# Kernel optimization log

Measured on AMD Instinct MI355X. Metric: run time of the kernel, lower is better.

The kernel has to match this reference:

```python
import jax, jax.numpy as jnp
import numpy as np


def _graph_conv(feat, W, b, src, dst, num_nodes):
    """DGL GraphConv with norm='both', activation=relu.
    out = relu(D_in^{-1/2} * A * D_out^{-1/2} * (X @ W) + b)
    Degrees are clamped to a minimum of 1 (DGL behavior).
    """
    # Linear transform first (d_in == d_out here, order is math-equivalent)
    h = feat @ W  # [N, d_out]
    ones = jnp.ones(src.shape[0], dtype=feat.dtype)
    out_deg = jnp.clip(jax.ops.segment_sum(ones, src, num_segments=num_nodes), 1.0)
    in_deg = jnp.clip(jax.ops.segment_sum(ones, dst, num_segments=num_nodes), 1.0)
    norm_src = jax.lax.rsqrt(out_deg)  # [N]
    norm_dst = jax.lax.rsqrt(in_deg)   # [N]
    # gather messages from source nodes, scaled by src norm
    msg = h[src] * norm_src[src][:, None]  # [E, d_out]
    agg = jax.ops.segment_sum(msg, dst, num_segments=num_nodes)  # [N, d_out]
    return jax.nn.relu(agg * norm_dst[:, None] + b)


def setup_inputs() -> dict:
    key = jax.random.key(0)
    ks = jax.random.split(key, 8)
    N = 50000
    E_c, E_d = 1600000, 800000
    d_c, d_d = 128, 256
    feat_c = jax.random.normal(ks[0], (N, d_c), dtype=jnp.float32)
    feat_d = jax.random.normal(ks[1], (N, d_d), dtype=jnp.float32)
    src_c = jax.random.randint(ks[2], (E_c,), 0, N, dtype=jnp.int32)
    dst_c = jax.random.randint(ks[3], (E_c,), 0, N, dtype=jnp.int32)
    src_d = jax.random.randint(ks[4], (E_d,), 0, N, dtype=jnp.int32)
    dst_d = jax.random.randint(ks[5], (E_d,), 0, N, dtype=jnp.int32)
    W_c = jax.random.normal(ks[6], (d_c, d_c), dtype=jnp.float32) * (1.0 / np.sqrt(d_c))
    W_d = jax.random.normal(ks[7], (d_d, d_d), dtype=jnp.float32) * (1.0 / np.sqrt(d_d))
    b_c = jnp.zeros((d_c,), dtype=jnp.float32)
    b_d = jnp.zeros((d_d,), dtype=jnp.float32)
    return {"feat_c": feat_c, "feat_d": feat_d, "src_c": src_c, "dst_c": dst_c,
            "src_d": src_d, "dst_d": dst_d, "W_c": W_c, "b_c": b_c,
            "W_d": W_d, "b_d": b_d}


def reference(feat_c, feat_d, src_c, dst_c, src_d, dst_d, W_c, b_c, W_d, b_d):
    N_c = feat_c.shape[0]
    N_d = feat_d.shape[0]
    homo_feature_c = _graph_conv(feat_c, W_c, b_c, src_c, dst_c, N_c)
    homo_feature_d = _graph_conv(feat_d, W_d, b_d, src_d, dst_d, N_d)
    return (homo_feature_c, homo_feature_d)
```

## Files before the change

kernel.cpp:

```cpp
#include <hip/hip_runtime.h>
#include <hip/hip_bf16.h>


typedef __attribute__((ext_vector_type(8))) short short8;
typedef __attribute__((ext_vector_type(4))) float f32x4;

#define RND 4096
#define CAPMAX 8960

static __device__ __forceinline__ ushort f2b(float f) {
    __hip_bfloat16 h = __float2bfloat16(f);
    return *reinterpret_cast<ushort*>(&h);
}
static __device__ __forceinline__ float b2f(ushort u) {
    union { unsigned int i; float f; } c;
    c.i = ((unsigned int)u) << 16;
    return c.f;
}
static __device__ __forceinline__ void gld_lds16(const void* g, void* l) {
    __builtin_amdgcn_global_load_lds(
        (const __attribute__((address_space(1))) unsigned int*)g,
        (__attribute__((address_space(3))) unsigned int*)l, 16, 0, 0);
}

__global__ __launch_bounds__(256) void part_kernel(
    const int* __restrict__ src_c, const int* __restrict__ dst_c, int Ec, int Rc,
    const int* __restrict__ src_d, const int* __restrict__ dst_d, int Ed, int Rd,
    int* gf_cd, int* gf_cs, int* gf_dd, int* gf_ds,
    int* dbuf_c, int* sbuf_c, int* dbuf_d, int* sbuf_d, int capc, int capd)
{
    __shared__ int pk[RND];
    __shared__ unsigned char pb[RND];
    __shared__ int hist[256], st[256], ex2[256], cur[256], gbase[256];

    const int tid = threadIdx.x;
    const int bid = blockIdx.x;
    const int* keys; const int* pays; int E; int* gf; int* buf; int cap; int e0;
    if (bid < Rc)            { keys = dst_c; pays = src_c; E = Ec; gf = gf_cd; buf = dbuf_c; cap = capc; e0 = bid * RND; }
    else if (bid < 2 * Rc)   { keys = src_c; pays = 0;     E = Ec; gf = gf_cs; buf = sbuf_c; cap = capc; e0 = (bid - Rc) * RND; }
    else if (bid < 2 * Rc + Rd) { keys = dst_d; pays = src_d; E = Ed; gf = gf_dd; buf = dbuf_d; cap = capd; e0 = (bid - 2 * Rc) * RND; }
    else                     { keys = src_d; pays = 0;     E = Ed; gf = gf_ds; buf = sbuf_d; cap = capd; e0 = (bid - 2 * Rc - Rd) * RND; }

    hist[tid] = 0;
    __syncthreads();

    int kb[RND / 256], pv[RND / 256];
    int n = 0;
#pragma unroll
    for (int r = 0; r < RND / 256; ++r) {
        int e = e0 + r * 256 + tid;
        if (e < E) {
            int k = keys[e];
            pv[r] = pays ? ((pays[e] << 8) | (k & 255)) : k;
            kb[r] = k >> 8;
            atomicAdd(&hist[kb[r]], 1);
            n = r + 1;
        }
    }
    __syncthreads();

    int x = hist[tid];
    st[tid] = x;
    __syncthreads();
    for (int off = 1; off < 256; off <<= 1) {
        int t2 = 0;
        if (tid >= off) t2 = st[tid - off];
        __syncthreads();
        if (tid >= off) st[tid] += t2;
        __syncthreads();
    }
    ex2[tid] = st[tid] - x;
    cur[tid] = st[tid] - x;
    __syncthreads();

    for (int r = 0; r < n; ++r) {
        int slot = atomicAdd(&cur[kb[r]], 1);
        pk[slot] = pv[r];
        pb[slot] = (unsigned char)kb[r];
    }
    if (x) gbase[tid] = atomicAdd(&gf[tid], x);
    __syncthreads();

    int m = st[255];
    for (int i = tid; i < m; i += 256) {
        int b = pb[i];
        int pos = gbase[b] + (i - ex2[b]);
        if (pos < cap) buf[(size_t)b * cap + pos] = pk[i];
    }
}

__global__ __launch_bounds__(256) void b2s_kernel(
    const int* __restrict__ sbuf_c, const int* __restrict__ gf_cs, int capc, int* cnt_c,
    const int* __restrict__ sbuf_d, const int* __restrict__ gf_ds, int capd, int* cnt_d,
    int N, int NBKT)
{
    __shared__ int h[256];
    const int tid = threadIdx.x;
    const int* sbuf; const int* gf; int cap; int* cnt; int bb;
    if ((int)blockIdx.x < NBKT) { sbuf = sbuf_c; gf = gf_cs; cap = capc; cnt = cnt_c; bb = blockIdx.x; }
    else { sbuf = sbuf_d; gf = gf_ds; cap = capd; cnt = cnt_d; bb = blockIdx.x - NBKT; }
    h[tid] = 0;
    __syncthreads();
    int m = gf[bb]; if (m > cap) m = cap;
    const int* reg = sbuf + (size_t)bb * cap;
    for (int i = tid; i < m; i += 256) atomicAdd(&h[reg[i] & 255], 1);
    __syncthreads();
    int v = bb * 256 + tid;
    if (v < N) cnt[v] = h[tid];
}

__global__ __launch_bounds__(256) void b2d_kernel(
    int* dbuf_c, const int* __restrict__ gf_cd, int capc, int* rs_c, int* dg_c,
    int* dbuf_d, const int* __restrict__ gf_dd, int capd, int* rs_d, int* dg_d,
    int N, int NBKT)
{
    __shared__ int pk[CAPMAX];
    __shared__ int h[256], st[256], ex2[256], cur[256];
    const int tid = threadIdx.x;
    int* bbuf; const int* gf; int cap; int* rs; int* dg; int bb;
    if ((int)blockIdx.x < NBKT) { bbuf = dbuf_c; gf = gf_cd; cap = capc; rs = rs_c; dg = dg_c; bb = blockIdx.x; }
    else { bbuf = dbuf_d; gf = gf_dd; cap = capd; rs = rs_d; dg = dg_d; bb = blockIdx.x - NBKT; }

    int m = gf[bb]; if (m > cap) m = cap;
    int* reg = bbuf + (size_t)bb * cap;

    h[tid] = 0;
    __syncthreads();
    for (int i = tid; i < m; i += 256) atomicAdd(&h[reg[i] & 255], 1);
    __syncthreads();
    int x = h[tid];
    st[tid] = x;
    __syncthreads();
    for (int off = 1; off < 256; off <<= 1) {
        int t2 = 0;
        if (tid >= off) t2 = st[tid - off];
        __syncthreads();
        if (tid >= off) st[tid] += t2;
        __syncthreads();
    }
    int ex_t = st[tid] - x;
    ex2[tid] = ex_t;
    cur[tid] = ex_t;
    int v = bb * 256 + tid;
    if (v < N) { rs[v] = bb * cap + ex_t; dg[v] = x; }
    __syncthreads();
    for (int i = tid; i < m; i += 256) {
        int p = reg[i];
        int slot = atomicAdd(&cur[p & 255], 1);
        pk[slot] = p >> 8;
    }
    __syncthreads();
    for (int i = tid; i < m; i += 256) reg[i] = pk[i];
}

__global__ __launch_bounds__(256) void wprep_kernel(
    const float* __restrict__ Wc, const float* __restrict__ Wd,
    ushort* __restrict__ Wtc, ushort* __restrict__ Wtd)
{
    int t = blockIdx.x * 256 + threadIdx.x;
    ushort o[8];
    if (t < 2048) {
        int n = t >> 4, slot = t & 15;
        int k0 = (slot ^ (n & 7)) << 3;
#pragma unroll
        for (int j = 0; j < 8; ++j) o[j] = f2b(Wc[(k0 + j) * 128 + n]);
        uint4 vv;
        vv.x = (unsigned)o[0] | ((unsigned)o[1] << 16);
        vv.y = (unsigned)o[2] | ((unsigned)o[3] << 16);
        vv.z = (unsigned)o[4] | ((unsigned)o[5] << 16);
        vv.w = (unsigned)o[6] | ((unsigned)o[7] << 16);
        *(uint4*)&Wtc[n * 128 + slot * 8] = vv;
    } else if (t < 2048 + 8192) {
        int tt = t - 2048;
        int ci = tt >> 11, r = tt & 2047;
        int n = r >> 3, slot = r & 7;
        int k0 = ci * 64 + ((slot ^ (n & 7)) << 3);
#pragma unroll
        for (int j = 0; j < 8; ++j) o[j] = f2b(Wd[(k0 + j) * 256 + n]);
        uint4 vv;
        vv.x = (unsigned)o[0] | ((unsigned)o[1] << 16);
        vv.y = (unsigned)o[2] | ((unsigned)o[3] << 16);
        vv.z = (unsigned)o[4] | ((unsigned)o[5] << 16);
        vv.w = (unsigned)o[6] | ((unsigned)o[7] << 16);
        *(uint4*)&Wtd[ci * 16384 + n * 64 + slot * 8] = vv;
    }
}

__global__ __launch_bounds__(256) void cast_kernel(
    const float* __restrict__ Xc, const int* __restrict__ coc, ushort* __restrict__ Xbc,
    const float* __restrict__ Xd, const int* __restrict__ cod, ushort* __restrict__ Xbd,
    int N, int nbc)
{
    const float* X; const int* co; ushort* Xb; int C4, t;
    if ((int)blockIdx.x < nbc) { X = Xc; co = coc; Xb = Xbc; C4 = 32; t = blockIdx.x * 256 + threadIdx.x; }
    else { X = Xd; co = cod; Xb = Xbd; C4 = 64; t = (blockIdx.x - nbc) * 256 + threadIdx.x; }
    if (t >= N * C4) return;
    int row = t / C4, c4 = t % C4;
    int od = co[row]; if (od < 1) od = 1;
    float nr = rsqrtf((float)od);
    float4 xv = ((const float4*)(X + (size_t)row * (C4 * 4)))[c4];
    ushort4 o;
    o.x = f2b(xv.x * nr); o.y = f2b(xv.y * nr);
    o.z = f2b(xv.z * nr); o.w = f2b(xv.w * nr);
    ((ushort4*)(Xb + (size_t)row * (C4 * 4)))[c4] = o;
}

template <int VEC>
static __device__ __forceinline__ void fused_branch(
    int blk, const ushort* __restrict__ Xb, const int* __restrict__ rs,
    const int* __restrict__ dg, const int* __restrict__ csr,
    const ushort* __restrict__ Wt, const float* __restrict__ bias,
    float* __restrict__ out, int N, ushort* At, ushort* Wls)
{
    constexpr int D = VEC * 64;
    constexpr int NCH = (D * D) / 16384;
    constexpr int BK = D / NCH;
    constexpr int NC = D / 64;
    const int tid = threadIdx.x;
    const int lane = tid & 63, wid = tid >> 6;

#pragma unroll
    for (int it = 0; it < 4; ++it) {
        int off16 = it * 512 + tid;
        gld_lds16(&Wt[off16 * 8], &Wls[off16 * 8]);
    }

    const int node0 = blk * 32;
#pragma unroll
    for (int s = 0; s < 4; ++s) {
        const int row = wid * 4 + s;
        const int v = node0 + row;
        float acc[VEC];
#pragma unroll
        for (int k = 0; k < VEC; ++k) acc[k] = 0.f;
        int deg = 0;
        if (v < N) {
            deg = dg[v];
            const int* rowp = csr + rs[v];
            for (int base = 0; base < deg; base += 64) {
                int m = deg - base; if (m > 64) m = 64;
                int u_l = (lane < m) ? rowp[base + lane] : 0;
#pragma unroll 8
                for (int j = 0; j < m; ++j) {
                    int u = __shfl(u_l, j);
                    const ushort* xr = Xb + (size_t)u * D + lane * VEC;
                    if constexpr (VEC == 2) {
                        unsigned int xv = *(const unsigned int*)xr;
                        acc[0] += b2f((ushort)(xv & 0xffff));
                        acc[1] += b2f((ushort)(xv >> 16));
                    } else {
                        uint2 xv = *(const uint2*)xr;
                        acc[0] += b2f((ushort)(xv.x & 0xffff));
                        acc[1] += b2f((ushort)(xv.x >> 16));
                        acc[2] += b2f((ushort)(xv.y & 0xffff));
                        acc[3] += b2f((ushort)(xv.y >> 16));
                    }
                }
            }
        }
        float nd = rsqrtf((float)(deg < 1 ? 1 : deg));
        const int k0 = lane * VEC;
        const int slot = (k0 >> 3) ^ (row & 7);
        ushort* dstp = &At[row * D + slot * 8 + (k0 & 7)];
        if constexpr (VEC == 2) {
            unsigned int pk = (unsigned)f2b(acc[0] * nd) | ((unsigned)f2b(acc[1] * nd) << 16);
            *(unsigned int*)dstp = pk;
        } else {
            uint2 pk;
            pk.x = (unsigned)f2b(acc[0] * nd) | ((unsigned)f2b(acc[1] * nd) << 16);
            pk.y = (unsigned)f2b(acc[2] * nd) | ((unsigned)f2b(acc[3] * nd) << 16);
            *(uint2*)dstp = pk;
        }
    }
    __syncthreads();

    const int wr = wid >> 2, wc = wid & 3;
    const int lr = lane & 15, lk8 = (lane >> 4) * 8;
    f32x4 acc[NC];
#pragma unroll
    for (int nc = 0; nc < NC; ++nc) acc[nc] = (f32x4)0.f;

#pragma unroll
    for (int ci = 0; ci < NCH; ++ci) {
        if (ci) {
            __syncthreads();
#pragma unroll
            for (int it = 0; it < 4; ++it) {
                int off16 = it * 512 + tid;
                gld_lds16(&Wt[ci * 16384 + off16 * 8], &Wls[off16 * 8]);
            }
            __syncthreads();
        }
#pragma unroll
        for (int k0 = 0; k0 < BK; k0 += 32) {
            const int r = wr * 16 + lr;
            const int kg = ci * BK + k0 + lk8;
            const int aslot = (kg >> 3) ^ (r & 7);
            short8 a = *(const short8*)&At[r * D + aslot * 8];
#pragma unroll
            for (int nc = 0; nc < NC; ++nc) {
                const int n = wc * (NC * 16) + nc * 16 + lr;
                const int kk = k0 + lk8;
                const int bslot = (kk >> 3) ^ (n & 7);
                short8 b = *(const short8*)&Wls[n * BK + bslot * 8];
                acc[nc] = __builtin_amdgcn_mfma_f32_16x16x32_bf16(a, b, acc[nc], 0, 0, 0);
            }
        }
    }

#pragma unroll
    for (int nc = 0; nc < NC; ++nc) {
        const int col = wc * (NC * 16) + nc * 16 + lr;
        const float bv = bias[col];
#pragma unroll
        for (int r4 = 0; r4 < 4; ++r4) {
            const int row = wr * 16 + (lane >> 4) * 4 + r4;
            const int v = node0 + row;
            if (v < N)
                out[(size_t)v * D + col] = fmaxf(acc[nc][r4] + bv, 0.f);
        }
    }
}

__global__ __launch_bounds__(512) void fused_kernel(
    const ushort* __restrict__ Xbc, const int* __restrict__ rsc,
    const int* __restrict__ dgc, const int* __restrict__ csrc,
    const ushort* __restrict__ Wtc, const float* __restrict__ bc, float* outc,
    const ushort* __restrict__ Xbd, const int* __restrict__ rsd,
    const int* __restrict__ dgd, const int* __restrict__ csrd,
    const ushort* __restrict__ Wtd, const float* __restrict__ bd, float* outd,
    int N, int nblkc)
{
    __shared__ ushort At[32 * 256];
    __shared__ ushort Wls[16384];
    if ((int)blockIdx.x < nblkc)
        fused_branch<2>(blockIdx.x, Xbc, rsc, dgc, csrc, Wtc, bc, outc, N, At, Wls);
    else
        fused_branch<4>(blockIdx.x - nblkc, Xbd, rsd, dgd, csrd, Wtd, bd, outd, N, At, Wls);
}

extern "C" void kernel_launch(void* const* d_in, const int* in_sizes, int n_in,
                              void* d_out, int out_size, void* d_ws, size_t ws_size,
                              hipStream_t stream)
{
    const float* feat_c = (const float*)d_in[0];
    const float* feat_d = (const float*)d_in[1];
    const int* src_c = (const int*)d_in[2];
    const int* dst_c = (const int*)d_in[3];
    const int* src_d = (const int*)d_in[4];
    const int* dst_d = (const int*)d_in[5];
    const float* W_c = (const float*)d_in[6];
    const float* b_c = (const float*)d_in[7];
    const float* W_d = (const float*)d_in[8];
    const float* b_d = (const float*)d_in[9];

    const int D_c = in_sizes[7];
    const int D_d = in_sizes[9];
    const int N = in_sizes[0] / D_c;
    const int E_c = in_sizes[2];
    const int E_d = in_sizes[4];

    float* out_c = (float*)d_out;
    float* out_d = (float*)d_out + (size_t)N * D_c;

    const int NBKT = (N + 255) >> 8;
    int capc = E_c / NBKT; capc += 8 * (int)sqrtf((float)capc) + 32; capc = (capc + 15) & ~15;
    int capd = E_d / NBKT; capd += 8 * (int)sqrtf((float)capd) + 32; capd = (capd + 15) & ~15;
    if (capc > CAPMAX) capc = CAPMAX;
    if (capd > CAPMAX) capd = CAPMAX;

    int* ws = (int*)d_ws;
    int* cnt_out_c = ws;
    int* cnt_out_d = ws + N;
    int* gf_cd = ws + 2 * (size_t)N;
    int* gf_cs = gf_cd + 256;
    int* gf_dd = gf_cs + 256;
    int* gf_ds = gf_dd + 256;
    int* rs_c  = gf_ds + 256;
    int* dg_c  = rs_c + N;
    int* rs_d  = dg_c + N;
    int* dg_d  = rs_d + N;
    ushort* Wt_c = (ushort*)(dg_d + N);
    ushort* Wt_d = Wt_c + 16384;
    int* dbuf_c = (int*)(Wt_d + 65536);
    int* sbuf_c = dbuf_c + (size_t)NBKT * capc;
    int* dbuf_d = sbuf_c + (size_t)NBKT * capc;
    int* sbuf_d = dbuf_d + (size_t)NBKT * capd;
    ushort* Xb_c = (ushort*)(sbuf_d + (size_t)NBKT * capd);
    ushort* Xb_d = Xb_c + (size_t)N * D_c;

    hipMemsetAsync(gf_cd, 0, 1024 * sizeof(int), stream);

    wprep_kernel<<<40, 256, 0, stream>>>(W_c, W_d, Wt_c, Wt_d);

    const int Rc = (E_c + RND - 1) / RND;
    const int Rd = (E_d + RND - 1) / RND;
    part_kernel<<<2 * (Rc + Rd), 256, 0, stream>>>(
        src_c, dst_c, E_c, Rc, src_d, dst_d, E_d, Rd,
        gf_cd, gf_cs, gf_dd, gf_ds,
        dbuf_c, sbuf_c, dbuf_d, sbuf_d, capc, capd);

    b2s_kernel<<<2 * NBKT, 256, 0, stream>>>(
        sbuf_c, gf_cs, capc, cnt_out_c,
        sbuf_d, gf_ds, capd, cnt_out_d, N, NBKT);

    int nbc = (N * (D_c / 4) + 255) / 256, nbd = (N * (D_d / 4) + 255) / 256;
    cast_kernel<<<nbc + nbd, 256, 0, stream>>>(feat_c, cnt_out_c, Xb_c,
                                               feat_d, cnt_out_d, Xb_d, N, nbc);

    b2d_kernel<<<2 * NBKT, 256, 0, stream>>>(
        dbuf_c, gf_cd, capc, rs_c, dg_c,
        dbuf_d, gf_dd, capd, rs_d, dg_d, N, NBKT);

    const int nblk = (N + 31) / 32;
    fused_kernel<<<2 * nblk, 512, 0, stream>>>(
        Xb_c, rs_c, dg_c, dbuf_c, Wt_c, b_c, out_c,
        Xb_d, rs_d, dg_d, dbuf_d, Wt_d, b_d, out_d, N, nblk);
}
```

Measured before the change: 442.9 us.

## Tile weight staging into 64x128 chunks to halve LDS footprint

Weight matrices are now pre-packed into 8192-element tiles of 64 K-rows by 128 output columns, so the fused kernel's shared weight buffer shrinks from 32 KB to 16 KB. The GEMM loop walks output-column chunks and K-chunks tile by tile. The smaller LDS footprint is meant to let more blocks reside per CU and hide the gather latency of the aggregation phase. In exchange, each block does more tile reloads and __syncthreads barriers, most of all in the 256-wide branch, which now loads 8 tiles instead of 4.

```diff
diff --git a/kernel.cpp b/kernel.cpp
--- a/kernel.cpp
+++ b/kernel.cpp
@@ -158,32 +158,23 @@
     ushort* __restrict__ Wtc, ushort* __restrict__ Wtd)
 {
     int t = blockIdx.x * 256 + threadIdx.x;
+    const float* W; ushort* Wt; int BN, tile, idx;
+    if (t < 2048)        { W = Wc; Wt = Wtc; BN = 128; tile = t >> 10; idx = t & 1023; }
+    else if (t < 10240)  { int tt = t - 2048; W = Wd; Wt = Wtd; BN = 256; tile = tt >> 10; idx = tt & 1023; }
+    else return;
+    int np = idx >> 3, slot = idx & 7;
+    int ch = tile >> 2, ci = tile & 3;
+    int k0 = ci * 64 + ((slot ^ (np & 7)) << 3);
+    int ncol = ch * 128 + np;
     ushort o[8];
-    if (t < 2048) {
-        int n = t >> 4, slot = t & 15;
-        int k0 = (slot ^ (n & 7)) << 3;
-#pragma unroll
-        for (int j = 0; j < 8; ++j) o[j] = f2b(Wc[(k0 + j) * 128 + n]);
-        uint4 vv;
-        vv.x = (unsigned)o[0] | ((unsigned)o[1] << 16);
-        vv.y = (unsigned)o[2] | ((unsigned)o[3] << 16);
-        vv.z = (unsigned)o[4] | ((unsigned)o[5] << 16);
-        vv.w = (unsigned)o[6] | ((unsigned)o[7] << 16);
-        *(uint4*)&Wtc[n * 128 + slot * 8] = vv;
-    } else if (t < 2048 + 8192) {
-        int tt = t - 2048;
-        int ci = tt >> 11, r = tt & 2047;
-        int n = r >> 3, slot = r & 7;
-        int k0 = ci * 64 + ((slot ^ (n & 7)) << 3);
-#pragma unroll
-        for (int j = 0; j < 8; ++j) o[j] = f2b(Wd[(k0 + j) * 256 + n]);
-        uint4 vv;
-        vv.x = (unsigned)o[0] | ((unsigned)o[1] << 16);
-        vv.y = (unsigned)o[2] | ((unsigned)o[3] << 16);
-        vv.z = (unsigned)o[4] | ((unsigned)o[5] << 16);
-        vv.w = (unsigned)o[6] | ((unsigned)o[7] << 16);
-        *(uint4*)&Wtd[ci * 16384 + n * 64 + slot * 8] = vv;
-    }
+#pragma unroll
+    for (int j = 0; j < 8; ++j) o[j] = f2b(W[(size_t)(k0 + j) * BN + ncol]);
+    uint4 vv;
+    vv.x = (unsigned)o[0] | ((unsigned)o[1] << 16);
+    vv.y = (unsigned)o[2] | ((unsigned)o[3] << 16);
+    vv.z = (unsigned)o[4] | ((unsigned)o[5] << 16);
+    vv.w = (unsigned)o[6] | ((unsigned)o[7] << 16);
+    *(uint4*)&Wt[tile * 8192 + np * 64 + slot * 8] = vv;
 }
 
 __global__ __launch_bounds__(256) void cast_kernel(
@@ -213,14 +204,13 @@
     float* __restrict__ out, int N, ushort* At, ushort* Wls)
 {
     constexpr int D = VEC * 64;
-    constexpr int NCH = (D * D) / 16384;
-    constexpr int BK = D / NCH;
-    constexpr int NC = D / 64;
+    constexpr int CH = VEC / 2;
+    constexpr int KCH = VEC;
     const int tid = threadIdx.x;
     const int lane = tid & 63, wid = tid >> 6;
 
 #pragma unroll
-    for (int it = 0; it < 4; ++it) {
+    for (int it = 0; it < 2; ++it) {
         int off16 = it * 512 + tid;
         gld_lds16(&Wt[off16 * 8], &Wls[off16 * 8]);
     }
@@ -276,50 +266,58 @@
 
     const int wr = wid >> 2, wc = wid & 3;
     const int lr = lane & 15, lk8 = (lane >> 4) * 8;
-    f32x4 acc[NC];
-#pragma unroll
-    for (int nc = 0; nc < NC; ++nc) acc[nc] = (f32x4)0.f;
-
-#pragma unroll
-    for (int ci = 0; ci < NCH; ++ci) {
-        if (ci) {
-            __syncthreads();
-#pragma unroll
-            for (int it = 0; it < 4; ++it) {
-                int off16 = it * 512 + tid;
-                gld_lds16(&Wt[ci * 16384 + off16 * 8], &Wls[off16 * 8]);
+    f32x4 acc[CH][2];
+#pragma unroll
+    for (int ch = 0; ch < CH; ++ch)
+#pragma unroll
+        for (int nc = 0; nc < 2; ++nc) acc[ch][nc] = (f32x4)0.f;
+
+#pragma unroll
+    for (int ch = 0; ch < CH; ++ch) {
+#pragma unroll
+        for (int ci = 0; ci < KCH; ++ci) {
+            const int tile = ch * KCH + ci;
+            if (tile) {
+                __syncthreads();
+#pragma unroll
+                for (int it = 0; it < 2; ++it) {
+                    int off16 = it * 512 + tid;
+                    gld_lds16(&Wt[tile * 8192 + off16 * 8], &Wls[off16 * 8]);
+                }
+                __syncthreads();
             }
-            __syncthreads();
-        }
-#pragma unroll
-        for (int k0 = 0; k0 < BK; k0 += 32) {
-            const int r = wr * 16 + lr;
-            const int kg = ci * BK + k0 + lk8;
-            const int aslot = (kg >> 3) ^ (r & 7);
-            short8 a = *(const short8*)&At[r * D + aslot * 8];
-#pragma unroll
-            for (int nc = 0; nc < NC; ++nc) {
-                const int n = wc * (NC * 16) + nc * 16 + lr;
-                const int kk = k0 + lk8;
-                const int bslot = (kk >> 3) ^ (n & 7);
-                short8 b = *(const short8*)&Wls[n * BK + bslot * 8];
-                acc[nc] = __builtin_amdgcn_mfma_f32_16x16x32_bf16(a, b, acc[nc], 0, 0, 0);
+#pragma unroll
+            for (int k0 = 0; k0 < 64; k0 += 32) {
+                const int r = wr * 16 + lr;
+                const int kg = ci * 64 + k0 + lk8;
+                const int aslot = (kg >> 3) ^ (r & 7);
+                short8 a = *(const short8*)&At[r * D + aslot * 8];
+#pragma unroll
+                for (int nc = 0; nc < 2; ++nc) {
+                    const int np = wc * 32 + nc * 16 + lr;
+                    const int kk = k0 + lk8;
+                    const int bslot = (kk >> 3) ^ (np & 7);
+                    short8 b = *(const short8*)&Wls[np * 64 + bslot * 8];
+                    acc[ch][nc] = __builtin_amdgcn_mfma_f32_16x16x32_bf16(a, b, acc[ch][nc], 0, 0, 0);
+                }
             }
         }
     }
 
 #pragma unroll
-    for (int nc = 0; nc < NC; ++nc) {
-        const int col = wc * (NC * 16) + nc * 16 + lr;
-        const float bv = bias[col];
-#pragma unroll
-        for (int r4 = 0; r4 < 4; ++r4) {
-            const int row = wr * 16 + (lane >> 4) * 4 + r4;
-            const int v = node0 + row;
-            if (v < N)
-                out[(size_t)v * D + col] = fmaxf(acc[nc][r4] + bv, 0.f);
+    for (int ch = 0; ch < CH; ++ch)
+#pragma unroll
+        for (int nc = 0; nc < 2; ++nc) {
+            const int col = ch * 128 + wc * 32 + nc * 16 + lr;
+            const float bv = bias[col];
+#pragma unroll
+            for (int r4 = 0; r4 < 4; ++r4) {
+                const int row = wr * 16 + (lane >> 4) * 4 + r4;
+                const int v = node0 + row;
+                if (v < N)
+                    out[(size_t)v * D + col] = fmaxf(acc[ch][nc][r4] + bv, 0.f);
+            }
         }
-    }
 }
 
 __global__ __launch_bounds__(512) void fused_kernel(
@@ -332,7 +330,7 @@
     int N, int nblkc)
 {
     __shared__ ushort At[32 * 256];
-    __shared__ ushort Wls[16384];
+    __shared__ ushort Wls[8192];
     if ((int)blockIdx.x < nblkc)
         fused_branch<2>(blockIdx.x, Xbc, rsc, dgc, csrc, Wtc, bc, outc, N, At, Wls);
     else
```

Measured after the change: 402.7 us. 9.1% less time.
